# Kernel optimization log

Measured on AMD Instinct MI355X. Metric: run time of the kernel, lower is better.

Reference implementation:

```python
import jax, jax.numpy as jnp
import numpy as np
from jax import lax

B_, L_, D_ = 4, 3136, 256
DH, DS, DR = 256, 16, 16  # d_inner//2, d_state, dt_rank (ceil(256/16))


def _ln(x, g, b):
    m = x.mean(-1, keepdims=True)
    v = ((x - m) ** 2).mean(-1, keepdims=True)
    return (x - m) * lax.rsqrt(v + 1e-5) * g + b


def _dwconv_same(x, w):
    # x: (B, C, L), w: (C, 1, K) depthwise, padding='same', no bias
    return lax.conv_general_dilated(x, w, (1,), 'SAME',
        dimension_numbers=('NCH', 'OIH', 'NCH'), feature_group_count=x.shape[1])


def _selective_scan(u, delta, A, Bm, Cm, Dp, delta_bias):
    # u, delta: (b, d, l); A: (d, n); Bm, Cm: (b, n, l)
    delta = jax.nn.softplus(delta + delta_bias[None, :, None])
    dA = jnp.exp(jnp.einsum('bdl,dn->lbdn', delta, A))          # (l,b,d,n)
    dBu = jnp.einsum('bdl,bnl,bdl->lbdn', delta, Bm, u)          # (l,b,d,n)
    C_l = jnp.transpose(Cm, (2, 0, 1))                           # (l,b,n)
    h0 = jnp.zeros(dA.shape[1:], u.dtype)

    def step(h, inp):
        dA_t, dBu_t, C_t = inp
        h = dA_t * h + dBu_t
        return h, jnp.einsum('bdn,bn->bd', h, C_t)

    _, ys = lax.scan(step, h0, (dA, dBu, C_l))                   # ys: (l,b,d)
    return jnp.transpose(ys, (1, 2, 0)) + u * Dp[None, :, None]


def _mamba(x, in_proj_w, conv_x_w, conv_z_w, x_proj_w, dt_proj_w, dt_proj_b, A_log, Dp, out_proj_w):
    xz = jnp.einsum('bld,ed->bel', x, in_proj_w)                 # (b, 2*DH, l)
    xb, zb = xz[:, :DH], xz[:, DH:]
    xb = jax.nn.silu(_dwconv_same(xb, conv_x_w))
    zb = jax.nn.silu(_dwconv_same(zb, conv_z_w))
    x_dbl = jnp.einsum('bdl,ed->ble', xb, x_proj_w)              # (b, l, DR+2*DS)
    dt, Bm, Cm = x_dbl[..., :DR], x_dbl[..., DR:DR + DS], x_dbl[..., DR + DS:]
    delta = jnp.einsum('blr,dr->bdl', dt, dt_proj_w)             # (b, DH, l)
    Bm = jnp.transpose(Bm, (0, 2, 1))                            # (b, DS, l)
    Cm = jnp.transpose(Cm, (0, 2, 1))
    A = -jnp.exp(A_log)
    y = _selective_scan(xb, delta, A, Bm, Cm, Dp, dt_proj_b)     # (b, DH, l)
    y = jnp.concatenate([y, zb], axis=1)                         # (b, 2*DH, l)
    return jnp.einsum('bel,de->bld', y, out_proj_w)


def _block(x, ln1_g, ln1_b, ln2_g, ln2_b, in_proj_w, conv_x_w, conv_z_w,
           x_proj_w, dt_proj_w, dt_proj_b, A_log, Dp, out_proj_w,
           mlp_w1, mlp_b1, mlp_w2, mlp_b2):
    x = x + _mamba(_ln(x, ln1_g, ln1_b), in_proj_w, conv_x_w, conv_z_w,
                   x_proj_w, dt_proj_w, dt_proj_b, A_log, Dp, out_proj_w)
    h = _ln(x, ln2_g, ln2_b)
    h = jax.nn.gelu(jnp.einsum('bld,hd->blh', h, mlp_w1) + mlp_b1, approximate=False)
    return x + (jnp.einsum('blh,dh->bld', h, mlp_w2) + mlp_b2)


def setup_inputs() -> dict:
    key = jax.random.key(0)
    ks = jax.random.split(key, 12)
    f = lambda k, s, sc=0.02: jax.random.normal(k, s, dtype=jnp.float32) * sc
    dt = jnp.exp(jax.random.uniform(ks[9], (DH,), dtype=jnp.float32)
                 * (np.log(0.1) - np.log(0.001)) + np.log(0.001))
    dt = jnp.clip(dt, 1e-4)
    inv_dt = dt + jnp.log(-jnp.expm1(-dt))
    return {
        'x': jax.random.normal(ks[0], (B_, L_, D_), dtype=jnp.float32),
        'ln1_g': jnp.ones((D_,), jnp.float32), 'ln1_b': jnp.zeros((D_,), jnp.float32),
        'ln2_g': jnp.ones((D_,), jnp.float32), 'ln2_b': jnp.zeros((D_,), jnp.float32),
        'in_proj_w': f(ks[1], (2 * DH, D_)),
        'conv_x_w': f(ks[2], (DH, 1, 3), 0.1),
        'conv_z_w': f(ks[3], (DH, 1, 3), 0.1),
        'x_proj_w': f(ks[4], (DR + 2 * DS, DH)),
        'dt_proj_w': f(ks[5], (DH, DR), DR ** -0.5),
        'dt_proj_b': inv_dt,
        'A_log': jnp.log(jnp.tile(jnp.arange(1, DS + 1, dtype=jnp.float32)[None, :], (DH, 1))),
        'Dp': jnp.ones((DH,), jnp.float32),
        'out_proj_w': f(ks[6], (D_, 2 * DH)),
        'mlp_w1': f(ks[7], (4 * D_, D_)), 'mlp_b1': jnp.zeros((4 * D_,), jnp.float32),
        'mlp_w2': f(ks[8], (D_, 4 * D_)), 'mlp_b2': jnp.zeros((D_,), jnp.float32),
    }


def reference(x, ln1_g, ln1_b, ln2_g, ln2_b, in_proj_w, conv_x_w, conv_z_w,
              x_proj_w, dt_proj_w, dt_proj_b, A_log, Dp, out_proj_w,
              mlp_w1, mlp_b1, mlp_w2, mlp_b2):
    return _block(x, ln1_g, ln1_b, ln2_g, ln2_b, in_proj_w, conv_x_w, conv_z_w,
                  x_proj_w, dt_proj_w, dt_proj_b, A_log, Dp, out_proj_w,
                  mlp_w1, mlp_b1, mlp_w2, mlp_b2)
```

## Files before the change

kernel.cpp:

```cpp
#include <hip/hip_runtime.h>
#include <hip/hip_bf16.h>

#define B_ 4
#define L_ 3136
#define D_ 256
#define NCH 49
#define LCH 64
#define M_ (B_*L_)

__device__ __forceinline__ float bf2f(unsigned short u) {
    union { unsigned int i; float f; } v; v.i = ((unsigned int)u) << 16; return v.f;
}
__device__ __forceinline__ unsigned short f2bs(float f) {
    __hip_bfloat16 h = __float2bfloat16(f);
    return *(unsigned short*)&h;
}
__device__ __forceinline__ float ldw(const void* p, size_t i, bool bf) {
    return bf ? bf2f(((const unsigned short*)p)[i]) : ((const float*)p)[i];
}
__device__ __forceinline__ void cvt4(ushort4 a, float* o) {
    o[0] = bf2f(a.x); o[1] = bf2f(a.y); o[2] = bf2f(a.z); o[3] = bf2f(a.w);
}
__device__ __forceinline__ void cvt8g(const unsigned short* p, bool v, float* o) {
    if (v) {
        ushort4 a = *(const ushort4*)p;
        ushort4 b = *(const ushort4*)(p + 4);
        cvt4(a, o); cvt4(b, o + 4);
    } else {
        #pragma unroll
        for (int i = 0; i < 8; ++i) o[i] = 0.f;
    }
}
__device__ __forceinline__ float dpp_add_xor1(float x) {
    int m = __builtin_amdgcn_update_dpp(0, __float_as_int(x), 0xB1, 0xF, 0xF, true);
    return x + __int_as_float(m);
}
__device__ __forceinline__ float dpp_add_xor2(float x) {
    int m = __builtin_amdgcn_update_dpp(0, __float_as_int(x), 0x4E, 0xF, 0xF, true);
    return x + __int_as_float(m);
}

__global__ __launch_bounds__(256) void detect_kernel(
    const unsigned int* __restrict__ xw, int* __restrict__ flag)
{
    int t = threadIdx.x; int cnt = 0;
    for (int i = t; i < 2048; i += 256) {
        unsigned int lo = xw[i] & 0xFFFFu;
        unsigned int e = (lo >> 7) & 0xFFu;
        if (e >= 0x58u && e <= 0x97u) cnt++;
    }
    #pragma unroll
    for (int o = 32; o > 0; o >>= 1) cnt += __shfl_down(cnt, o);
    __shared__ int sred[4];
    if ((t & 63) == 0) sred[t >> 6] = cnt;
    __syncthreads();
    if (t == 0) flag[0] = (sred[0] + sred[1] + sred[2] + sred[3] > 1024) ? 1 : 0;
}

__global__ __launch_bounds__(256) void ln_kernel(
    const void* __restrict__ xin, int inmode,
    const void* __restrict__ g, const void* __restrict__ bsh,
    unsigned short* __restrict__ out, const int* __restrict__ flagp)
{
    const bool wbf = (*flagp != 0);
    const bool inbf = (inmode < 0) ? wbf : true;
    int row = blockIdx.x * 4 + (threadIdx.x >> 6);
    int lane = threadIdx.x & 63;
    size_t idx = (size_t)row * 256 + lane * 4;
    float v[4];
    if (inbf) {
        ushort4 a = *(const ushort4*)((const unsigned short*)xin + idx);
        cvt4(a, v);
    } else {
        float4 a = *(const float4*)((const float*)xin + idx);
        v[0] = a.x; v[1] = a.y; v[2] = a.z; v[3] = a.w;
    }
    float s = v[0] + v[1] + v[2] + v[3];
    float s2 = v[0]*v[0] + v[1]*v[1] + v[2]*v[2] + v[3]*v[3];
    #pragma unroll
    for (int o = 32; o > 0; o >>= 1) { s += __shfl_xor(s, o); s2 += __shfl_xor(s2, o); }
    float mean = s * (1.f / 256.f);
    float var  = s2 * (1.f / 256.f) - mean * mean;
    float rs = rsqrtf(var + 1e-5f);
    ushort4 o;
    o.x = f2bs((v[0] - mean) * rs * ldw(g, lane*4+0, wbf) + ldw(bsh, lane*4+0, wbf));
    o.y = f2bs((v[1] - mean) * rs * ldw(g, lane*4+1, wbf) + ldw(bsh, lane*4+1, wbf));
    o.z = f2bs((v[2] - mean) * rs * ldw(g, lane*4+2, wbf) + ldw(bsh, lane*4+2, wbf));
    o.w = f2bs((v[3] - mean) * rs * ldw(g, lane*4+3, wbf) + ldw(bsh, lane*4+3, wbf));
    *(ushort4*)(out + idx) = o;
}

enum { EPI_NONE = 0, EPI_SP = 1, EPI_RES = 2, EPI_GELU = 3, EPI_OUT = 4 };

typedef __attribute__((ext_vector_type(8))) short bf16x8;
typedef __attribute__((ext_vector_type(4))) float f32x4;

__device__ __forceinline__ void gload_lds16(const void* g, void* l) {
    __builtin_amdgcn_global_load_lds(
        (const __attribute__((address_space(1))) unsigned int*)g,
        (__attribute__((address_space(3))) unsigned int*)l, 16, 0, 0);
}

template<int EPI>
__global__ __launch_bounds__(256) void mgemm_kernel(
    const unsigned short* __restrict__ A, const unsigned short* __restrict__ A2, int Ksplit,
    const void* __restrict__ W, void* __restrict__ Cout,
    int N, int K, int lda, int ldc,
    const void* __restrict__ bias, const void* __restrict__ resb,
    const unsigned short* __restrict__ resf, const int* __restrict__ flagp)
{
    const bool wbf = (*flagp != 0);
    __shared__ unsigned short As[2][64][64];
    __shared__ unsigned short Ws[2][64][64];
    const int tid = threadIdx.x;

    const int nwg = gridDim.x * gridDim.y;
    int bid = blockIdx.y * gridDim.x + blockIdx.x;
    int wgid = ((nwg & 7) == 0) ? ((bid & 7) * (nwg >> 3) + (bid >> 3)) : bid;
    const int bx = wgid % gridDim.x;
    const int by = wgid / gridDim.x;
    const int bm = by * 64, bn = bx * 64;

    const int l = tid & 63, wid = tid >> 6;
    const int wr = wid >> 1, wc = wid & 1;
    const int lr = l & 15;
    const int lq = l >> 4;
    const int srow = tid >> 3;
    const int sblk = ((tid & 7) ^ (srow & 7)) * 8;
    const int dcol = (tid & 7) * 8;

    f32x4 acc[2][2] = {};
    const int NT = K >> 6;

    auto stage = [&](int buf, int k0s) {
        const unsigned short* Ab; int kc;
        if (k0s < Ksplit) { Ab = A;  kc = k0s; }
        else              { Ab = A2; kc = k0s - Ksplit; }
        gload_lds16(Ab + (size_t)(bm + srow) * lda + kc + sblk,      &As[buf][srow][dcol]);
        gload_lds16(Ab + (size_t)(bm + 32 + srow) * lda + kc + sblk, &As[buf][32 + srow][dcol]);
        if (wbf) {
            const unsigned short* Wb = (const unsigned short*)W;
            gload_lds16(Wb + (size_t)(bn + srow) * K + k0s + sblk,      &Ws[buf][srow][dcol]);
            gload_lds16(Wb + (size_t)(bn + 32 + srow) * K + k0s + sblk, &Ws[buf][32 + srow][dcol]);
        } else {
            const float* Wf = (const float*)W;
            #pragma unroll
            for (int h = 0; h < 2; ++h) {
                int row = h * 32 + srow;
                const float* p = Wf + (size_t)(bn + row) * K + k0s + (tid & 7) * 8;
                float4 w0 = *(const float4*)p;
                float4 w1 = *(const float4*)(p + 4);
                ushort4 o0, o1;
                o0.x = f2bs(w0.x); o0.y = f2bs(w0.y); o0.z = f2bs(w0.z); o0.w = f2bs(w0.w);
                o1.x = f2bs(w1.x); o1.y = f2bs(w1.y); o1.z = f2bs(w1.z); o1.w = f2bs(w1.w);
                *(ushort4*)&Ws[buf][row][sblk]     = o0;
                *(ushort4*)&Ws[buf][row][sblk + 4] = o1;
            }
        }
    };

    stage(0, 0);
    asm volatile("s_waitcnt vmcnt(0)" ::: "memory");
    __syncthreads();

    int cur = 0;
    for (int kt = 0; kt < NT; ++kt) {
        if (kt + 1 < NT) stage(cur ^ 1, (kt + 1) << 6);

        bf16x8 af[2][2], bfr[2][2];
        #pragma unroll
        for (int i = 0; i < 2; ++i) {
            #pragma unroll
            for (int ks = 0; ks < 2; ++ks) {
                int ca = ((ks * 4 + lq) ^ (lr & 7)) * 8;
                af[i][ks]  = *(const bf16x8*)&As[cur][wr * 32 + i * 16 + lr][ca];
                bfr[i][ks] = *(const bf16x8*)&Ws[cur][wc * 32 + i * 16 + lr][ca];
            }
        }
        #pragma unroll
        for (int ks = 0; ks < 2; ++ks)
            #pragma unroll
            for (int i = 0; i < 2; ++i)
                #pragma unroll
                for (int j = 0; j < 2; ++j)
                    acc[i][j] = __builtin_amdgcn_mfma_f32_16x16x32_bf16(af[i][ks], bfr[j][ks], acc[i][j], 0, 0, 0);

        if (kt + 1 < NT) {
            asm volatile("s_waitcnt vmcnt(0)" ::: "memory");
            __syncthreads();
            cur ^= 1;
        }
    }

    #pragma unroll
    for (int i = 0; i < 2; ++i) {
        #pragma unroll
        for (int j = 0; j < 2; ++j) {
            const int col = bn + wc * 32 + j * 16 + lr;
            #pragma unroll
            for (int e = 0; e < 4; ++e) {
                const int row = bm + wr * 32 + i * 16 + lq * 4 + e;
                float t = acc[i][j][e];
                if (EPI == EPI_RES) {
                    t += ldw(resb, (size_t)row * 256 + col, wbf);
                } else if (EPI == EPI_GELU) {
                    t += ldw(bias, col, wbf);
                    t = 0.5f * t * (1.f + erff(t * 0.70710678118654752f));
                } else if (EPI == EPI_OUT) {
                    t += ldw(bias, col, wbf) + bf2f(resf[(size_t)row * 256 + col]);
                }
                if (EPI == EPI_OUT && !wbf) {
                    ((float*)Cout)[(size_t)row * ldc + col] = t;
                } else {
                    ((unsigned short*)Cout)[(size_t)row * ldc + col] = f2bs(t);
                }
            }
        }
    }
}

__global__ __launch_bounds__(256) void xproj_kernel(
    const unsigned short* __restrict__ A, const void* __restrict__ W,
    float* __restrict__ Cout, const int* __restrict__ flagp)
{
    const bool wbf = (*flagp != 0);
    __shared__ unsigned short As[2][64][64];
    __shared__ unsigned short Ws[2][64][64];
    const int tid = threadIdx.x;
    const int bm = blockIdx.y * 64;

    const int l = tid & 63, wid = tid >> 6;
    const int wr = wid >> 1, wc = wid & 1;
    const int lr = l & 15, lq = l >> 4;
    const int srow = tid >> 3;
    const int sblk = ((tid & 7) ^ (srow & 7)) * 8;
    const int dcol = (tid & 7) * 8;

    {
        ushort4 zz4; zz4.x = 0; zz4.y = 0; zz4.z = 0; zz4.w = 0;
        int buf = tid >> 7, rr = 48 + ((tid >> 3) & 15), cc = (tid & 7) * 8;
        *(ushort4*)&Ws[buf][rr][cc] = zz4;
        *(ushort4*)&Ws[buf][rr][cc + 4] = zz4;
    }
    __syncthreads();

    f32x4 acc[2][2] = {};

    auto stage = [&](int buf, int k0s) {
        gload_lds16(A + (size_t)(bm + srow) * 256 + k0s + sblk,      &As[buf][srow][dcol]);
        gload_lds16(A + (size_t)(bm + 32 + srow) * 256 + k0s + sblk, &As[buf][32 + srow][dcol]);
        if (wbf) {
            const unsigned short* Wb = (const unsigned short*)W;
            gload_lds16(Wb + (size_t)srow * 256 + k0s + sblk, &Ws[buf][srow][dcol]);
            if (srow < 16)
                gload_lds16(Wb + (size_t)(32 + srow) * 256 + k0s + sblk, &Ws[buf][32 + srow][dcol]);
        } else {
            const float* Wf = (const float*)W;
            #pragma unroll
            for (int h = 0; h < 2; ++h) {
                int row = h * 32 + srow;
                if (row < 48) {
                    const float* p = Wf + (size_t)row * 256 + k0s + (tid & 7) * 8;
                    float4 w0 = *(const float4*)p;
                    float4 w1 = *(const float4*)(p + 4);
                    ushort4 o0, o1;
                    o0.x = f2bs(w0.x); o0.y = f2bs(w0.y); o0.z = f2bs(w0.z); o0.w = f2bs(w0.w);
                    o1.x = f2bs(w1.x); o1.y = f2bs(w1.y); o1.z = f2bs(w1.z); o1.w = f2bs(w1.w);
                    *(ushort4*)&Ws[buf][row][sblk]     = o0;
                    *(ushort4*)&Ws[buf][row][sblk + 4] = o1;
                }
            }
        }
    };

    stage(0, 0);
    asm volatile("s_waitcnt vmcnt(0)" ::: "memory");
    __syncthreads();

    int cur = 0;
    for (int kt = 0; kt < 4; ++kt) {
        if (kt + 1 < 4) stage(cur ^ 1, (kt + 1) << 6);
        bf16x8 af[2][2], bfr[2][2];
        #pragma unroll
        for (int i = 0; i < 2; ++i) {
            #pragma unroll
            for (int ks = 0; ks < 2; ++ks) {
                int ca = ((ks * 4 + lq) ^ (lr & 7)) * 8;
                af[i][ks]  = *(const bf16x8*)&As[cur][wr * 32 + i * 16 + lr][ca];
                bfr[i][ks] = *(const bf16x8*)&Ws[cur][wc * 32 + i * 16 + lr][ca];
            }
        }
        #pragma unroll
        for (int ks = 0; ks < 2; ++ks)
            #pragma unroll
            for (int i = 0; i < 2; ++i)
                #pragma unroll
                for (int j = 0; j < 2; ++j)
                    acc[i][j] = __builtin_amdgcn_mfma_f32_16x16x32_bf16(af[i][ks], bfr[j][ks], acc[i][j], 0, 0, 0);
        if (kt + 1 < 4) {
            asm volatile("s_waitcnt vmcnt(0)" ::: "memory");
            __syncthreads();
            cur ^= 1;
        }
    }

    #pragma unroll
    for (int i = 0; i < 2; ++i) {
        #pragma unroll
        for (int j = 0; j < 2; ++j) {
            const int col = wc * 32 + j * 16 + lr;
            if (col < 48) {
                #pragma unroll
                for (int e = 0; e < 4; ++e) {
                    const int row = bm + wr * 32 + i * 16 + lq * 4 + e;
                    Cout[(size_t)row * 48 + col] = acc[i][j][e];
                }
            }
        }
    }
}

__global__ __launch_bounds__(256) void dtgemm_kernel(
    const float* __restrict__ Axd, const void* __restrict__ W,
    unsigned short* __restrict__ Cout, const void* __restrict__ bias,
    const int* __restrict__ flagp)
{
    const bool wbf = (*flagp != 0);
    __shared__ unsigned short Ah[64][16];
    __shared__ unsigned short Al[64][16];
    __shared__ unsigned short Wb[64][16];
    const int tid = threadIdx.x;
    const int nwg = gridDim.x * gridDim.y;
    int bid = blockIdx.y * gridDim.x + blockIdx.x;
    int wgid = ((nwg & 7) == 0) ? ((bid & 7) * (nwg >> 3) + (bid >> 3)) : bid;
    const int bx = wgid % gridDim.x, by = wgid / gridDim.x;
    const int bm = by * 64, bn = bx * 64;

    {
        int rr = tid >> 2, cc = (tid & 3) * 4;
        float4 v = *(const float4*)(Axd + (size_t)(bm + rr) * 48 + cc);
        float vv[4] = {v.x, v.y, v.z, v.w};
        ushort4 hi4, lo4;
        unsigned short* hp = (unsigned short*)&hi4;
        unsigned short* lp = (unsigned short*)&lo4;
        #pragma unroll
        for (int j = 0; j < 4; ++j) {
            unsigned short h = f2bs(vv[j]);
            hp[j] = h;
            lp[j] = f2bs(vv[j] - bf2f(h));
        }
        *(ushort4*)&Ah[rr][cc] = hi4;
        *(ushort4*)&Al[rr][cc] = lo4;
        ushort4 wb4;
        unsigned short* wp = (unsigned short*)&wb4;
        if (wbf) {
            wb4 = *(const ushort4*)((const unsigned short*)W + (size_t)(bn + rr) * 16 + cc);
        } else {
            float4 wv = *(const float4*)((const float*)W + (size_t)(bn + rr) * 16 + cc);
            wp[0] = f2bs(wv.x); wp[1] = f2bs(wv.y); wp[2] = f2bs(wv.z); wp[3] = f2bs(wv.w);
        }
        *(ushort4*)&Wb[rr][cc] = wb4;
    }
    __syncthreads();

    const int l = tid & 63, wid = tid >> 6;
    const int wr = wid >> 1, wc = wid & 1;
    const int lr = l & 15, lq = l >> 4;

    f32x4 acc[2][2] = {};
    bf16x8 ah[2], al8[2], wb8[2];
    #pragma unroll
    for (int i = 0; i < 2; ++i) { ah[i] = bf16x8{}; al8[i] = bf16x8{}; wb8[i] = bf16x8{}; }
    if (lq < 2) {
        #pragma unroll
        for (int i = 0; i < 2; ++i) {
            ah[i]  = *(const bf16x8*)&Ah[wr * 32 + i * 16 + lr][lq * 8];
            al8[i] = *(const bf16x8*)&Al[wr * 32 + i * 16 + lr][lq * 8];
            wb8[i] = *(const bf16x8*)&Wb[wc * 32 + i * 16 + lr][lq * 8];
        }
    }
    #pragma unroll
    for (int i = 0; i < 2; ++i)
        #pragma unroll
        for (int j = 0; j < 2; ++j) {
            acc[i][j] = __builtin_amdgcn_mfma_f32_16x16x32_bf16(ah[i],  wb8[j], acc[i][j], 0, 0, 0);
            acc[i][j] = __builtin_amdgcn_mfma_f32_16x16x32_bf16(al8[i], wb8[j], acc[i][j], 0, 0, 0);
        }

    #pragma unroll
    for (int i = 0; i < 2; ++i) {
        #pragma unroll
        for (int j = 0; j < 2; ++j) {
            const int col = bn + wc * 32 + j * 16 + lr;
            #pragma unroll
            for (int e = 0; e < 4; ++e) {
                const int row = bm + wr * 32 + i * 16 + lq * 4 + e;
                float t = acc[i][j][e] + ldw(bias, col, wbf);
                t = (t > 20.f) ? t : log1pf(__expf(t));
                Cout[(size_t)row * 256 + col] = f2bs(t);
            }
        }
    }
}

__global__ __launch_bounds__(256) void conv_silu_kernel(
    const unsigned short* __restrict__ xz,
    const void* __restrict__ wx, const void* __restrict__ wz,
    unsigned short* __restrict__ u, unsigned short* __restrict__ z,
    const int* __restrict__ flagp)
{
    const bool wbf = (*flagp != 0);
    int sub = threadIdx.x >> 5;
    int cb = (threadIdx.x & 31) * 8;
    int bl = blockIdx.x * 8 + sub;
    int l = bl % L_;
    const unsigned short* r = xz + (size_t)bl * 512;
    bool hasm = (l > 0), hasp = (l < L_ - 1);

    float wxa[24], wza[24];
    if (wbf) {
        const unsigned short* px = (const unsigned short*)wx + 3 * cb;
        const unsigned short* pz = (const unsigned short*)wz + 3 * cb;
        #pragma unroll
        for (int t = 0; t < 3; ++t) {
            cvt4(*(const ushort4*)(px + t * 8), &wxa[t * 8]);
            cvt4(*(const ushort4*)(px + t * 8 + 4), &wxa[t * 8 + 4]);
            cvt4(*(const ushort4*)(pz + t * 8), &wza[t * 8]);
            cvt4(*(const ushort4*)(pz + t * 8 + 4), &wza[t * 8 + 4]);
        }
    } else {
        const float* px = (const float*)wx + 3 * cb;
        const float* pz = (const float*)wz + 3 * cb;
        #pragma unroll
        for (int t = 0; t < 6; ++t) {
            *(float4*)&wxa[t * 4] = *(const float4*)(px + t * 4);
            *(float4*)&wza[t * 4] = *(const float4*)(pz + t * 4);
        }
    }

    float xm[8], xc[8], xp[8];
    cvt8g(r + cb - 512, hasm, xm);
    cvt8g(r + cb,       true, xc);
    cvt8g(r + cb + 512, hasp, xp);
    ushort4 o0, o1;
    {
        unsigned short* op = (unsigned short*)&o0;
        unsigned short* op1 = (unsigned short*)&o1;
        #pragma unroll
        for (int j = 0; j < 8; ++j) {
            float v = xm[j] * wxa[3 * j] + xc[j] * wxa[3 * j + 1] + xp[j] * wxa[3 * j + 2];
            v = v / (1.f + __expf(-v));
            if (j < 4) op[j] = f2bs(v); else op1[j - 4] = f2bs(v);
        }
    }
    *(ushort4*)(u + (size_t)bl * 256 + cb) = o0;
    *(ushort4*)(u + (size_t)bl * 256 + cb + 4) = o1;

    cvt8g(r + cb - 256,  hasm, xm);
    cvt8g(r + 256 + cb,  true, xc);
    cvt8g(r + 768 + cb,  hasp, xp);
    {
        unsigned short* op = (unsigned short*)&o0;
        unsigned short* op1 = (unsigned short*)&o1;
        #pragma unroll
        for (int j = 0; j < 8; ++j) {
            float v = xm[j] * wza[3 * j] + xc[j] * wza[3 * j + 1] + xp[j] * wza[3 * j + 2];
            v = v / (1.f + __expf(-v));
            if (j < 4) op[j] = f2bs(v); else op1[j - 4] = f2bs(v);
        }
    }
    *(ushort4*)(z + (size_t)bl * 256 + cb) = o0;
    *(ushort4*)(z + (size_t)bl * 256 + cb + 4) = o1;
}

__global__ __launch_bounds__(256) void scan_a_kernel(
    const unsigned short* __restrict__ delta, const unsigned short* __restrict__ u,
    const float* __restrict__ xdbl, const void* __restrict__ A_log,
    float* __restrict__ hend, float* __restrict__ dsum, const int* __restrict__ flagp)
{
    const bool wbf = (*flagp != 0);
    int blk = blockIdx.x;
    int b = blk / (NCH * 16);
    int rem = blk % (NCH * 16);
    int c = rem / 16, db = rem % 16;

    __shared__ unsigned int sdu[64][16];
    __shared__ float sB[64][16];

    const unsigned short* dp = delta + (size_t)b * L_ * 256;
    const unsigned short* up = u     + (size_t)b * L_ * 256;
    const float* xd = xdbl + (size_t)b * L_ * 48;

    int r = threadIdx.x >> 2, q = (threadIdx.x & 3) * 4;
    int lrow = c * 64 + r;
    {
        ushort4 dv = *(const ushort4*)(dp + (size_t)lrow * 256 + db * 16 + q);
        ushort4 uv = *(const ushort4*)(up + (size_t)lrow * 256 + db * 16 + q);
        uint4 pk;
        pk.x = (unsigned int)dv.x | ((unsigned int)uv.x << 16);
        pk.y = (unsigned int)dv.y | ((unsigned int)uv.y << 16);
        pk.z = (unsigned int)dv.z | ((unsigned int)uv.z << 16);
        pk.w = (unsigned int)dv.w | ((unsigned int)uv.w << 16);
        *(uint4*)&sdu[r][q] = pk;
        *(float4*)&sB[r][q] = *(const float4*)(xd + (size_t)lrow * 48 + 16 + q);
    }
    __syncthreads();

    int g = threadIdx.x >> 4, n = threadIdx.x & 15;
    int d = db * 16 + g;
    float An2 = -__expf(ldw(A_log, d * 16 + n, wbf)) * 1.44269504088896f;
    float h = 0.f, s = 0.f;
    #pragma unroll 8
    for (int t2 = 0; t2 < 64; ++t2) {
        unsigned int du = sdu[t2][g];
        float ds = __uint_as_float(du << 16);
        float ut = __uint_as_float(du & 0xFFFF0000u);
        float Bn = sB[t2][n];
        float e = exp2f(ds * An2);
        h = fmaf(e, h, ds * ut * Bn);
        s += ds;
    }
    size_t pair = (size_t)b * 256 + d;
    hend[(pair * NCH + c) * 16 + n] = h;
    if (n == 0) dsum[pair * NCH + c] = s;
}

__global__ __launch_bounds__(256) void scan_b_kernel(
    const void* __restrict__ A_log, float* __restrict__ hend,
    const float* __restrict__ dsum, const int* __restrict__ flagp)
{
    const bool wbf = (*flagp != 0);
    int gid = blockIdx.x * 256 + threadIdx.x;
    int pair = gid >> 4, n = gid & 15;
    int d = pair & 255;
    float An = -__expf(ldw(A_log, d * 16 + n, wbf));
    float H = 0.f;
    #pragma unroll 7
    for (int c = 0; c < NCH; ++c) {
        size_t idx = ((size_t)pair * NCH + c) * 16 + n;
        float he = hend[idx];
        hend[idx] = H;
        H = __expf(An * dsum[(size_t)pair * NCH + c]) * H + he;
    }
}

__global__ __launch_bounds__(256) void scan_c_kernel(
    const unsigned short* __restrict__ delta, const unsigned short* __restrict__ u,
    const float* __restrict__ xdbl, const void* __restrict__ A_log,
    const void* __restrict__ Dp, const float* __restrict__ hinit,
    unsigned short* __restrict__ y, const int* __restrict__ flagp)
{
    const bool wbf = (*flagp != 0);
    int blk = blockIdx.x;
    int b = blk / (NCH * 16);
    int rem = blk % (NCH * 16);
    int c = rem / 16, db = rem % 16;

    __shared__ unsigned int sdu[64][16];
    __shared__ float sBC[64][16][2];
    __shared__ float syp[64][16][4];
    __shared__ unsigned short sy[64][16];

    const unsigned short* dp = delta + (size_t)b * L_ * 256;
    const unsigned short* up = u     + (size_t)b * L_ * 256;
    const float* xd = xdbl + (size_t)b * L_ * 48;

    int r = threadIdx.x >> 2, q = (threadIdx.x & 3) * 4;
    int lrow = c * 64 + r;
    {
        ushort4 dv = *(const ushort4*)(dp + (size_t)lrow * 256 + db * 16 + q);
        ushort4 uv = *(const ushort4*)(up + (size_t)lrow * 256 + db * 16 + q);
        uint4 pk;
        pk.x = (unsigned int)dv.x | ((unsigned int)uv.x << 16);
        pk.y = (unsigned int)dv.y | ((unsigned int)uv.y << 16);
        pk.z = (unsigned int)dv.z | ((unsigned int)uv.z << 16);
        pk.w = (unsigned int)dv.w | ((unsigned int)uv.w << 16);
        *(uint4*)&sdu[r][q] = pk;
        float4 Bv = *(const float4*)(xd + (size_t)lrow * 48 + 16 + q);
        float4 Cv = *(const float4*)(xd + (size_t)lrow * 48 + 32 + q);
        float2 p0; p0.x = Bv.x; p0.y = Cv.x; *(float2*)&sBC[r][q + 0][0] = p0;
        float2 p1; p1.x = Bv.y; p1.y = Cv.y; *(float2*)&sBC[r][q + 1][0] = p1;
        float2 p2; p2.x = Bv.z; p2.y = Cv.z; *(float2*)&sBC[r][q + 2][0] = p2;
        float2 p3; p3.x = Bv.w; p3.y = Cv.w; *(float2*)&sBC[r][q + 3][0] = p3;
    }
    __syncthreads();

    int g = threadIdx.x >> 4, n = threadIdx.x & 15;
    int d = db * 16 + g;
    float An2 = -__expf(ldw(A_log, d * 16 + n, wbf)) * 1.44269504088896f;
    size_t pair = (size_t)b * 256 + d;
    float h = hinit[(pair * NCH + c) * 16 + n];
    const bool wlane = ((n & 3) == 0);
    #pragma unroll 4
    for (int t2 = 0; t2 < 64; ++t2) {
        unsigned int du = sdu[t2][g];
        float ds = __uint_as_float(du << 16);
        float ut = __uint_as_float(du & 0xFFFF0000u);
        float2 bc = *(const float2*)&sBC[t2][n][0];
        float e = exp2f(ds * An2);
        h = fmaf(e, h, ds * ut * bc.x);
        float yp = h * bc.y;
        yp = dpp_add_xor1(yp);
        yp = dpp_add_xor2(yp);
        if (wlane) syp[t2][g][n >> 2] = yp;
    }
    __syncthreads();

    #pragma unroll
    for (int cc = 0; cc < 4; ++cc) {
        int cell = threadIdx.x + cc * 256;
        int t2 = cell >> 4, gg = cell & 15;
        float4 p = *(const float4*)&syp[t2][gg][0];
        unsigned int du = sdu[t2][gg];
        float ut = __uint_as_float(du & 0xFFFF0000u);
        float Dd = ldw(Dp, db * 16 + gg, wbf);
        sy[t2][gg] = f2bs(p.x + p.y + p.z + p.w + ut * Dd);
    }
    __syncthreads();
    *(ushort4*)(y + ((size_t)b * L_ + c * 64 + r) * 256 + db * 16 + q) = *(ushort4*)&sy[r][q];
}

extern "C" void kernel_launch(void* const* d_in, const int* in_sizes, int n_in,
                              void* d_out, int out_size, void* d_ws, size_t ws_size,
                              hipStream_t stream) {
    const void* x         = d_in[0];
    const void* ln1_g     = d_in[1];
    const void* ln1_b     = d_in[2];
    const void* ln2_g     = d_in[3];
    const void* ln2_b     = d_in[4];
    const void* in_proj_w = d_in[5];
    const void* conv_x_w  = d_in[6];
    const void* conv_z_w  = d_in[7];
    const void* x_proj_w  = d_in[8];
    const void* dt_proj_w = d_in[9];
    const void* dt_proj_b = d_in[10];
    const void* A_log     = d_in[11];
    const void* Dp        = d_in[12];
    const void* out_proj_w= d_in[13];
    const void* mlp_w1    = d_in[14];
    const void* mlp_b1    = d_in[15];
    const void* mlp_w2    = d_in[16];
    const void* mlp_b2    = d_in[17];

    float* ws = (float*)d_ws;
    unsigned short* xz    = (unsigned short*)(ws);
    unsigned short* delta = (unsigned short*)(ws);
    unsigned short* yb    = (unsigned short*)(ws + 1605632);
    float*          xdbl  = ws + 3211264;
    float*          hend  = ws + 3813376;
    float*          dsum  = ws + 4616192;
    unsigned short* hmid  = (unsigned short*)(ws);
    unsigned short* ub    = (unsigned short*)(ws + 6422528);
    unsigned short* xres  = (unsigned short*)(ws + 6422528);
    unsigned short* xnb   = (unsigned short*)(ws + 8028160);
    int*            flag  = (int*)(ws + 9633792);

    dim3 blk(256);
    const int KNOSPLIT = 1 << 30;

    detect_kernel<<<1, blk, 0, stream>>>((const unsigned int*)x, flag);

    ln_kernel<<<M_ / 4, blk, 0, stream>>>(x, -1, ln1_g, ln1_b, xnb, flag);

    mgemm_kernel<EPI_NONE><<<dim3(8, 196), blk, 0, stream>>>(
        xnb, nullptr, KNOSPLIT, in_proj_w, xz, 512, 256, 256, 512, nullptr, nullptr, nullptr, flag);

    conv_silu_kernel<<<M_ / 8, blk, 0, stream>>>(xz, conv_x_w, conv_z_w, ub, xnb, flag);

    xproj_kernel<<<dim3(1, 196), blk, 0, stream>>>(ub, x_proj_w, xdbl, flag);

    dtgemm_kernel<<<dim3(4, 196), blk, 0, stream>>>(xdbl, dt_proj_w, delta, dt_proj_b, flag);

    scan_a_kernel<<<B_ * NCH * 16, blk, 0, stream>>>(delta, ub, xdbl, A_log, hend, dsum, flag);
    scan_b_kernel<<<64, blk, 0, stream>>>(A_log, hend, dsum, flag);
    scan_c_kernel<<<B_ * NCH * 16, blk, 0, stream>>>(delta, ub, xdbl, A_log, Dp, hend, yb, flag);

    mgemm_kernel<EPI_RES><<<dim3(4, 196), blk, 0, stream>>>(
        yb, xnb, 256, out_proj_w, xres, 256, 512, 256, 256, nullptr, x, nullptr, flag);

    ln_kernel<<<M_ / 4, blk, 0, stream>>>(xres, 1, ln2_g, ln2_b, xnb, flag);

    mgemm_kernel<EPI_GELU><<<dim3(16, 196), blk, 0, stream>>>(
        xnb, nullptr, KNOSPLIT, mlp_w1, hmid, 1024, 256, 256, 1024, mlp_b1, nullptr, nullptr, flag);

    mgemm_kernel<EPI_OUT><<<dim3(4, 196), blk, 0, stream>>>(
        hmid, nullptr, KNOSPLIT, mlp_w2, d_out, 256, 1024, 1024, 256, mlp_b2, nullptr, xres, flag);
}
```

Baseline: 297.2 us.

## Transpose scan shared-memory tiles for vector LDS reads and batch scan_b loads

Shared-memory staging in scan_a and scan_c is transposed and padded (stride 68/132), so each thread reads four timesteps per vector LDS load instead of one scalar load per step, and scan_c writes partial y sums as float4. scan_b now runs 64-thread blocks across 256 blocks and prefetches seven chunks of hend/dsum before its serial recurrence, so loads overlap with the exponential chain. The transposed writes during staging become scalar and strided, which may bring bank conflicts into the load phase.

```diff
diff --git a/kernel.cpp b/kernel.cpp
--- a/kernel.cpp
+++ b/kernel.cpp
@@ -484,8 +484,8 @@
     int rem = blk % (NCH * 16);
     int c = rem / 16, db = rem % 16;
 
-    __shared__ unsigned int sdu[64][16];
-    __shared__ float sB[64][16];
+    __shared__ unsigned int sduT[16][68];
+    __shared__ float sBT[16][68];
 
     const unsigned short* dp = delta + (size_t)b * L_ * 256;
     const unsigned short* up = u     + (size_t)b * L_ * 256;
@@ -496,13 +496,13 @@
     {
         ushort4 dv = *(const ushort4*)(dp + (size_t)lrow * 256 + db * 16 + q);
         ushort4 uv = *(const ushort4*)(up + (size_t)lrow * 256 + db * 16 + q);
-        uint4 pk;
-        pk.x = (unsigned int)dv.x | ((unsigned int)uv.x << 16);
-        pk.y = (unsigned int)dv.y | ((unsigned int)uv.y << 16);
-        pk.z = (unsigned int)dv.z | ((unsigned int)uv.z << 16);
-        pk.w = (unsigned int)dv.w | ((unsigned int)uv.w << 16);
-        *(uint4*)&sdu[r][q] = pk;
-        *(float4*)&sB[r][q] = *(const float4*)(xd + (size_t)lrow * 48 + 16 + q);
+        sduT[q + 0][r] = (unsigned)dv.x | ((unsigned)uv.x << 16);
+        sduT[q + 1][r] = (unsigned)dv.y | ((unsigned)uv.y << 16);
+        sduT[q + 2][r] = (unsigned)dv.z | ((unsigned)uv.z << 16);
+        sduT[q + 3][r] = (unsigned)dv.w | ((unsigned)uv.w << 16);
+        float4 Bv = *(const float4*)(xd + (size_t)lrow * 48 + 16 + q);
+        sBT[q + 0][r] = Bv.x; sBT[q + 1][r] = Bv.y;
+        sBT[q + 2][r] = Bv.z; sBT[q + 3][r] = Bv.w;
     }
     __syncthreads();
 
@@ -510,37 +510,49 @@
     int d = db * 16 + g;
     float An2 = -__expf(ldw(A_log, d * 16 + n, wbf)) * 1.44269504088896f;
     float h = 0.f, s = 0.f;
-    #pragma unroll 8
-    for (int t2 = 0; t2 < 64; ++t2) {
-        unsigned int du = sdu[t2][g];
-        float ds = __uint_as_float(du << 16);
-        float ut = __uint_as_float(du & 0xFFFF0000u);
-        float Bn = sB[t2][n];
-        float e = exp2f(ds * An2);
-        h = fmaf(e, h, ds * ut * Bn);
-        s += ds;
+    #pragma unroll 4
+    for (int tb = 0; tb < 16; ++tb) {
+        uint4 du4 = *(const uint4*)&sduT[g][tb * 4];
+        float4 B4 = *(const float4*)&sBT[n][tb * 4];
+        #pragma unroll
+        for (int j = 0; j < 4; ++j) {
+            unsigned du = (j == 0) ? du4.x : (j == 1) ? du4.y : (j == 2) ? du4.z : du4.w;
+            float Bn = (j == 0) ? B4.x : (j == 1) ? B4.y : (j == 2) ? B4.z : B4.w;
+            float ds = __uint_as_float(du << 16);
+            float ut = __uint_as_float(du & 0xFFFF0000u);
+            float e = exp2f(ds * An2);
+            h = fmaf(e, h, ds * ut * Bn);
+            s += ds;
+        }
     }
     size_t pair = (size_t)b * 256 + d;
     hend[(pair * NCH + c) * 16 + n] = h;
     if (n == 0) dsum[pair * NCH + c] = s;
 }
 
-__global__ __launch_bounds__(256) void scan_b_kernel(
+__global__ __launch_bounds__(64) void scan_b_kernel(
     const void* __restrict__ A_log, float* __restrict__ hend,
     const float* __restrict__ dsum, const int* __restrict__ flagp)
 {
     const bool wbf = (*flagp != 0);
-    int gid = blockIdx.x * 256 + threadIdx.x;
+    int gid = blockIdx.x * 64 + threadIdx.x;
     int pair = gid >> 4, n = gid & 15;
     int d = pair & 255;
     float An = -__expf(ldw(A_log, d * 16 + n, wbf));
     float H = 0.f;
-    #pragma unroll 7
-    for (int c = 0; c < NCH; ++c) {
-        size_t idx = ((size_t)pair * NCH + c) * 16 + n;
-        float he = hend[idx];
-        hend[idx] = H;
-        H = __expf(An * dsum[(size_t)pair * NCH + c]) * H + he;
+    #pragma unroll 1
+    for (int c0 = 0; c0 < NCH; c0 += 7) {
+        float he[7], dd[7];
+        #pragma unroll
+        for (int j = 0; j < 7; ++j) {
+            he[j] = hend[((size_t)pair * NCH + c0 + j) * 16 + n];
+            dd[j] = dsum[(size_t)pair * NCH + c0 + j];
+        }
+        #pragma unroll
+        for (int j = 0; j < 7; ++j) {
+            hend[((size_t)pair * NCH + c0 + j) * 16 + n] = H;
+            H = __expf(An * dd[j]) * H + he[j];
+        }
     }
 }
 
@@ -556,9 +568,9 @@
     int rem = blk % (NCH * 16);
     int c = rem / 16, db = rem % 16;
 
-    __shared__ unsigned int sdu[64][16];
-    __shared__ float sBC[64][16][2];
-    __shared__ float syp[64][16][4];
+    __shared__ unsigned int sduT[16][68];
+    __shared__ float sBCT[16][132];
+    __shared__ float sypT[16][4][68];
     __shared__ unsigned short sy[64][16];
 
     const unsigned short* dp = delta + (size_t)b * L_ * 256;
@@ -570,18 +582,16 @@
     {
         ushort4 dv = *(const ushort4*)(dp + (size_t)lrow * 256 + db * 16 + q);
         ushort4 uv = *(const ushort4*)(up + (size_t)lrow * 256 + db * 16 + q);
-        uint4 pk;
-        pk.x = (unsigned int)dv.x | ((unsigned int)uv.x << 16);
-        pk.y = (unsigned int)dv.y | ((unsigned int)uv.y << 16);
-        pk.z = (unsigned int)dv.z | ((unsigned int)uv.z << 16);
-        pk.w = (unsigned int)dv.w | ((unsigned int)uv.w << 16);
-        *(uint4*)&sdu[r][q] = pk;
+        sduT[q + 0][r] = (unsigned)dv.x | ((unsigned)uv.x << 16);
+        sduT[q + 1][r] = (unsigned)dv.y | ((unsigned)uv.y << 16);
+        sduT[q + 2][r] = (unsigned)dv.z | ((unsigned)uv.z << 16);
+        sduT[q + 3][r] = (unsigned)dv.w | ((unsigned)uv.w << 16);
         float4 Bv = *(const float4*)(xd + (size_t)lrow * 48 + 16 + q);
         float4 Cv = *(const float4*)(xd + (size_t)lrow * 48 + 32 + q);
-        float2 p0; p0.x = Bv.x; p0.y = Cv.x; *(float2*)&sBC[r][q + 0][0] = p0;
-        float2 p1; p1.x = Bv.y; p1.y = Cv.y; *(float2*)&sBC[r][q + 1][0] = p1;
-        float2 p2; p2.x = Bv.z; p2.y = Cv.z; *(float2*)&sBC[r][q + 2][0] = p2;
-        float2 p3; p3.x = Bv.w; p3.y = Cv.w; *(float2*)&sBC[r][q + 3][0] = p3;
+        float2 t0; t0.x = Bv.x; t0.y = Cv.x; *(float2*)&sBCT[q + 0][r * 2] = t0;
+        float2 t1; t1.x = Bv.y; t1.y = Cv.y; *(float2*)&sBCT[q + 1][r * 2] = t1;
+        float2 t2; t2.x = Bv.z; t2.y = Cv.z; *(float2*)&sBCT[q + 2][r * 2] = t2;
+        float2 t3; t3.x = Bv.w; t3.y = Cv.w; *(float2*)&sBCT[q + 3][r * 2] = t3;
     }
     __syncthreads();
 
@@ -591,18 +601,28 @@
     size_t pair = (size_t)b * 256 + d;
     float h = hinit[(pair * NCH + c) * 16 + n];
     const bool wlane = ((n & 3) == 0);
+    const int p = n >> 2;
     #pragma unroll 4
-    for (int t2 = 0; t2 < 64; ++t2) {
-        unsigned int du = sdu[t2][g];
-        float ds = __uint_as_float(du << 16);
-        float ut = __uint_as_float(du & 0xFFFF0000u);
-        float2 bc = *(const float2*)&sBC[t2][n][0];
-        float e = exp2f(ds * An2);
-        h = fmaf(e, h, ds * ut * bc.x);
-        float yp = h * bc.y;
-        yp = dpp_add_xor1(yp);
-        yp = dpp_add_xor2(yp);
-        if (wlane) syp[t2][g][n >> 2] = yp;
+    for (int tb = 0; tb < 16; ++tb) {
+        uint4 du4 = *(const uint4*)&sduT[g][tb * 4];
+        float4 bc01 = *(const float4*)&sBCT[n][tb * 8];
+        float4 bc23 = *(const float4*)&sBCT[n][tb * 8 + 4];
+        float yp4[4];
+        #pragma unroll
+        for (int j = 0; j < 4; ++j) {
+            unsigned du = (j == 0) ? du4.x : (j == 1) ? du4.y : (j == 2) ? du4.z : du4.w;
+            float Bn = (j == 0) ? bc01.x : (j == 1) ? bc01.z : (j == 2) ? bc23.x : bc23.z;
+            float Cn = (j == 0) ? bc01.y : (j == 1) ? bc01.w : (j == 2) ? bc23.y : bc23.w;
+            float ds = __uint_as_float(du << 16);
+            float ut = __uint_as_float(du & 0xFFFF0000u);
+            float e = exp2f(ds * An2);
+            h = fmaf(e, h, ds * ut * Bn);
+            float yp = h * Cn;
+            yp = dpp_add_xor1(yp);
+            yp = dpp_add_xor2(yp);
+            yp4[j] = yp;
+        }
+        if (wlane) *(float4*)&sypT[g][p][tb * 4] = *(float4*)yp4;
     }
     __syncthreads();
 
@@ -610,11 +630,11 @@
     for (int cc = 0; cc < 4; ++cc) {
         int cell = threadIdx.x + cc * 256;
         int t2 = cell >> 4, gg = cell & 15;
-        float4 p = *(const float4*)&syp[t2][gg][0];
-        unsigned int du = sdu[t2][gg];
+        float sum = sypT[gg][0][t2] + sypT[gg][1][t2] + sypT[gg][2][t2] + sypT[gg][3][t2];
+        unsigned du = sduT[gg][t2];
         float ut = __uint_as_float(du & 0xFFFF0000u);
         float Dd = ldw(Dp, db * 16 + gg, wbf);
-        sy[t2][gg] = f2bs(p.x + p.y + p.z + p.w + ut * Dd);
+        sy[t2][gg] = f2bs(sum + ut * Dd);
     }
     __syncthreads();
     *(ushort4*)(y + ((size_t)b * L_ + c * 64 + r) * 256 + db * 16 + q) = *(ushort4*)&sy[r][q];
@@ -672,7 +692,7 @@
     dtgemm_kernel<<<dim3(4, 196), blk, 0, stream>>>(xdbl, dt_proj_w, delta, dt_proj_b, flag);
 
     scan_a_kernel<<<B_ * NCH * 16, blk, 0, stream>>>(delta, ub, xdbl, A_log, hend, dsum, flag);
-    scan_b_kernel<<<64, blk, 0, stream>>>(A_log, hend, dsum, flag);
+    scan_b_kernel<<<256, dim3(64), 0, stream>>>(A_log, hend, dsum, flag);
     scan_c_kernel<<<B_ * NCH * 16, blk, 0, stream>>>(delta, ub, xdbl, A_log, Dp, hend, yb, flag);
 
     mgemm_kernel<EPI_RES><<<dim3(4, 196), blk, 0, stream>>>(
```

Result: no change. 296.7 us (median of 2 runs) (-0.2%).
